# Kernel optimization log

Measured on AMD Instinct MI355X. Metric: run time of the kernel, lower is better.

Reference implementation:

```python
import jax, jax.numpy as jnp
from jax import lax
import numpy as np

B, L, D, MD, H, R, T = 128, 128, 300, 50, 512, 128, 4
HD = H // 2          # per-direction GRU hidden
GIN = D + MD         # GRU input dim (word emb + mask emb)


def setup_inputs():
    key = jax.random.key(0)
    ks = jax.random.split(key, 16)
    s = 0.05
    sents = jax.random.normal(ks[0], (B, L, D), jnp.float32)
    lens = jnp.sort(jax.random.randint(ks[1], (B,), 96, L + 1))[::-1]  # sorted desc, like pack_padded
    j = jnp.arange(L)
    # aspect span: positions 5..7 are the target (contiguous ones, inside every lens)
    masks = ((j >= 5) & (j < 8)).astype(jnp.int32)[None, :] * jnp.ones((B, 1), jnp.int32)
    labels = jax.random.randint(ks[2], (B,), 0, 3)
    mask_table = jax.random.normal(ks[3], (2, MD)) * s
    gWihf = jax.random.normal(ks[4], (3 * HD, GIN)) * s
    gWhhf = jax.random.normal(ks[5], (3 * HD, HD)) * s
    gbihf = jnp.zeros((3 * HD,), jnp.float32)
    gbhhf = jnp.zeros((3 * HD,), jnp.float32)
    gWihb = jax.random.normal(ks[6], (3 * HD, GIN)) * s
    gWhhb = jax.random.normal(ks[7], (3 * HD, HD)) * s
    gbihb = jnp.zeros((3 * HD,), jnp.float32)
    gbhhb = jnp.zeros((3 * HD,), jnp.float32)
    hW = jax.random.normal(ks[8], (4, R, H)) * s   # 4 branch hNlinear weights [R,H]
    hb = jnp.zeros((4, R), jnp.float32)
    tW = jax.random.normal(ks[9], (4, T, R)) * s   # 4 branch feat2tri weights [T,R]
    tb = jnp.zeros((4, T), jnp.float32)
    trans = jax.random.normal(ks[10], (4, T, T)) * s  # 4 CRF transition matrices
    lW = jax.random.normal(ks[11], (3, 4 * H)) * s    # feat2label2
    lb = jnp.zeros((3,), jnp.float32)
    return {"sents": sents, "mask_table": mask_table,
            "gWihf": gWihf, "gWhhf": gWhhf, "gbihf": gbihf, "gbhhf": gbhhf,
            "gWihb": gWihb, "gWhhb": gWhhb, "gbihb": gbihb, "gbhhb": gbhhb,
            "hW": hW, "hb": hb, "tW": tW, "tb": tb, "trans": trans,
            "lW": lW, "lb": lb, "masks": masks, "lens": lens, "labels": labels}


def _gru_dir(x, valid, Wih, Whh, bih, bhh):
    # x: [B,L,GIN], valid: [B,L] bool. PyTorch GRU cell; padded steps emit 0 and keep hidden.
    gi_all = jnp.einsum('bld,gd->blg', x, Wih) + bih  # precompute input GEMM [B,L,3HD]

    def step(h, inp):
        gi, m = inp  # [B,3HD], [B]
        gh = h @ Whh.T + bhh
        ir, iz, inn = jnp.split(gi, 3, axis=-1)
        hr, hz, hn = jnp.split(gh, 3, axis=-1)
        r = jax.nn.sigmoid(ir + hr)
        z = jax.nn.sigmoid(iz + hz)
        n = jnp.tanh(inn + r * hn)
        hnew = (1.0 - z) * n + z * h
        h_carry = jnp.where(m[:, None], hnew, h)
        y = jnp.where(m[:, None], hnew, 0.0)
        return h_carry, y

    h0 = jnp.zeros((x.shape[0], HD), x.dtype)
    _, ys = lax.scan(step, h0, (gi_all.transpose(1, 0, 2), valid.T))
    return ys.transpose(1, 0, 2)  # [B,L,HD]


def _crf_marginals(feats, valid, trans):
    # feats: [B,L,T], valid: [B,L] bool, trans: [T,T]. Forward-backward marginals.
    fT = feats.transpose(1, 0, 2)  # [L,B,T]
    mT = valid.T                   # [L,B]

    def fwd(alpha, inp):
        f, m = inp
        new = jax.nn.logsumexp(alpha[:, :, None] + trans[None], axis=1) + f
        alpha = jnp.where(m[:, None], new, alpha)
        return alpha, alpha

    alpha0 = fT[0]
    _, alphas = lax.scan(fwd, alpha0, (fT[1:], mT[1:]))
    alphas = jnp.concatenate([alpha0[None], alphas], axis=0)  # [L,B,T]

    def bwd(beta, inp):
        f_next, m_next = inp
        new = jax.nn.logsumexp(trans[None] + (f_next + beta)[:, None, :], axis=2)
        beta = jnp.where(m_next[:, None], new, beta)
        return beta, beta

    beta_last = jnp.zeros_like(alpha0)
    _, betas = lax.scan(bwd, beta_last, (fT[1:], mT[1:]), reverse=True)
    betas = jnp.concatenate([betas, beta_last[None]], axis=0)  # [L,B,T]
    return jax.nn.softmax(alphas + betas, axis=-1).transpose(1, 0, 2)  # [B,L,T]


def _pos_weights(masks, lens):
    # replicates get_pos_weight
    j = jnp.arange(L)[None, :]
    begin = jnp.argmax(masks, axis=1)[:, None]
    tnum = jnp.sum(masks, axis=1)[:, None]
    lf = lens.astype(jnp.float32)[:, None]
    w = jnp.where(j < begin, 1.0 - (begin - j).astype(jnp.float32) / lf, 0.0)
    w = jnp.where(masks == 1, 1.0, w)
    w = jnp.where(j > begin + tnum, 1.0 - (j - begin).astype(jnp.float32) / lf, w)
    w = jnp.where(j > lens[:, None], 0.0, w)
    return w  # [B,L]


def _model(sents, mask_table, gWihf, gWhhf, gbihf, gbhhf, gWihb, gWhhb, gbihb, gbhhb,
           hW, hb, tW, tb, trans, lW, lb, masks, lens, labels):
    valid = jnp.arange(L)[None, :] < lens[:, None]  # [B,L]
    x = jnp.concatenate([sents, mask_table[masks]], axis=-1)  # [B,L,GIN]

    hf = _gru_dir(x, valid, gWihf, gWhhf, gbihf, gbhhf)
    # backward direction: reverse each sequence within its valid length
    j = jnp.arange(L)[None, :]
    rev_idx = jnp.clip(lens[:, None] - 1 - j, 0, L - 1)  # [B,L]
    x_rev = jnp.take_along_axis(x, rev_idx[:, :, None], axis=1)
    hb_rev = _gru_dir(x_rev, valid, gWihb, gWhhb, gbihb, gbhhb)
    hbk = jnp.take_along_axis(hb_rev, rev_idx[:, :, None], axis=1) * valid[:, :, None]

    ctx = jnp.concatenate([hf, hbk], axis=-1)  # [B,L,H]
    ctx = ctx * _pos_weights(masks, lens)[:, :, None]

    validf = valid.astype(ctx.dtype)
    svs = []
    for k in range(4):
        ck = jnp.einsum('blh,rh->blr', ctx, hW[k]) + hb[k]      # hNlinear
        fk = jnp.einsum('blr,tr->blt', ck, tW[k]) + tb[k]       # feat2triN
        marg = _crf_marginals(fk, valid, trans[k])
        sp = marg[:, :, 1] * validf                              # select tag-1 polarity in valid range
        sp = sp / jnp.sum(sp, axis=1, keepdims=True)             # normalize by gamma
        svs.append(jnp.einsum('bl,blh->bh', sp, ctx))            # weighted pooling

    sv = jax.nn.relu(jnp.concatenate(svs, axis=-1))  # [B,4H] (eval: dropout = identity)
    scores = sv @ lW.T + lb                          # [B,3]
    logp = jax.nn.log_softmax(scores, axis=1)
    cls_loss = -jnp.mean(logp[jnp.arange(B), labels])
    return cls_loss


def reference(sents, mask_table, gWihf, gWhhf, gbihf, gbhhf, gWihb, gWhhb, gbihb, gbhhb,
              hW, hb, tW, tb, trans, lW, lb, masks, lens, labels):
    return _model(sents, mask_table, gWihf, gWhhf, gbihf, gbhhf, gWihb, gWhhb, gbihb, gbhhb,
                  hW, hb, tW, tb, trans, lW, lb, masks, lens, labels)
```

## Files before the change

### kernel.cpp

```cpp
#include <hip/hip_runtime.h>
#include <hip/hip_bf16.h>

#define BB 128
#define LL 128
#define DD 300
#define MDIM 50
#define GINDIM 350
#define HDIM 256
#define G3 768
#define HH 512
#define RR 128
#define TT 4
#define NKB 4
#define MTOT (BB*LL)
#define N2 1536
#define KP 352

typedef __attribute__((ext_vector_type(8))) short short8;
typedef __attribute__((ext_vector_type(4))) float f32x4;

#define OFF_GI      0ull
#define OFF_CTXB    50331648ull
#define OFF_XBF     67108864ull
#define OFF_WIHB    78643200ull
#define OFF_WHHB    79724544ull
#define OFF_BIAS    80510976ull
#define OFF_W2      80517120ull
#define OFF_B2      80549888ull
#define OFF_BEG     80550144ull
#define OFF_TN      80550656ull
#define OFF_SCORES  80551168ull
#define OFF_FK      80553216ull
#define OFF_AL      81601792ull
#define OFF_SP      82650368ull
#define OFF_SPSUM   82912512ull
#define OFF_SV      82914560ull

__device__ __forceinline__ float sig_f(float x) { return 1.f / (1.f + __expf(-x)); }
__device__ __forceinline__ float tanh_f(float x) { float e = __expf(2.f * x); return 1.f - 2.f / (e + 1.f); }
__device__ __forceinline__ float b2f(unsigned short u) { return __uint_as_float(((unsigned)u) << 16); }

__global__ __launch_bounds__(256) void k_zero(float4* p) {
    size_t n4 = 16777216ull / 16;
    for (size_t i = blockIdx.x * 256ull + threadIdx.x; i < n4; i += (size_t)gridDim.x * 256ull)
        p[i] = make_float4(0.f, 0.f, 0.f, 0.f);
}

__global__ __launch_bounds__(256) void k_prep_x(const float* __restrict__ sents,
        const float* __restrict__ mask_table, const int* __restrict__ masks,
        __hip_bfloat16* __restrict__ xbf) {
    int idx = blockIdx.x * 256 + threadIdx.x;
    if (idx >= MTOT * KP) return;
    int m = idx / KP, k = idx % KP;
    float v = 0.f;
    if (k < DD) v = sents[(size_t)m * DD + k];
    else if (k < GINDIM) v = mask_table[masks[m] * MDIM + (k - DD)];
    xbf[idx] = __float2bfloat16(v);
}

__global__ __launch_bounds__(256) void k_prep_wihB(const float* __restrict__ Wf,
        const float* __restrict__ Wb, const float* __restrict__ bf_,
        const float* __restrict__ bb_, __hip_bfloat16* __restrict__ wihB,
        float* __restrict__ biasAll) {
    int idx = blockIdx.x * 256 + threadIdx.x;
    if (idx < N2 * KP) {
        int n = idx / KP, k = idx % KP;
        int dir = n >= G3; int g = n - dir * G3;
        const float* W = dir ? Wb : Wf;
        float v = (k < GINDIM) ? W[(size_t)g * GINDIM + k] : 0.f;
        wihB[idx] = __float2bfloat16(v);
    }
    if (idx < N2) biasAll[idx] = (idx < G3) ? bf_[idx] : bb_[idx - G3];
}

__global__ __launch_bounds__(256) void k_prep_whhB(const float* __restrict__ Wf,
        const float* __restrict__ Wb, __hip_bfloat16* __restrict__ whhB) {
    int idx = blockIdx.x * 256 + threadIdx.x;
    if (idx >= 2 * G3 * HDIM) return;
    int dir = idx / (G3 * HDIM);
    const float* W = dir ? Wb : Wf;
    whhB[idx] = __float2bfloat16(W[idx - dir * G3 * HDIM]);
}

__global__ __launch_bounds__(256) void k_prep_w2(const float* __restrict__ hW,
        const float* __restrict__ hb, const float* __restrict__ tW,
        const float* __restrict__ tb, float* __restrict__ W2, float* __restrict__ b2) {
    int idx = blockIdx.x * 256 + threadIdx.x;
    if (idx < 16 * HH) {
        int kt = idx >> 9, h = idx & 511;
        int k = kt >> 2, t = kt & 3;
        const float* tw = tW + (size_t)(k * TT + t) * RR;
        const float* hw = hW + (size_t)k * RR * HH + h;
        float acc = 0.f;
        #pragma unroll 4
        for (int r = 0; r < RR; ++r) acc += tw[r] * hw[(size_t)r * HH];
        W2[idx] = acc;
    }
    if (idx < 16) {
        int k = idx >> 2, t = idx & 3;
        const float* tw = tW + (size_t)(k * TT + t) * RR;
        const float* hbk = hb + k * RR;
        float acc = tb[k * TT + t];
        for (int r = 0; r < RR; ++r) acc += tw[r] * hbk[r];
        b2[idx] = acc;
    }
}

__global__ __launch_bounds__(128) void k_prep_bt(const int* __restrict__ masks,
        int* __restrict__ beg, int* __restrict__ tn) {
    int b = threadIdx.x;
    int best = masks[b * LL]; int idx = 0; int s = 0;
    for (int j = 0; j < LL; ++j) {
        int v = masks[b * LL + j]; s += v;
        if (v > best) { best = v; idx = j; }
    }
    beg[b] = idx; tn[b] = s;
}

__global__ __launch_bounds__(256) void k_mfma_gi(const short* __restrict__ xbf,
        const short* __restrict__ wihB, const float* __restrict__ biasAll,
        __hip_bfloat16* __restrict__ gi) {
    __shared__ short As[64][40];
    __shared__ short Bs[64][40];
    const int tid = threadIdx.x;
    const int m0 = blockIdx.y * 64, n0 = blockIdx.x * 64;
    const int w = tid >> 6, lane = tid & 63;
    const int srow = tid >> 2, skc = (tid & 3) * 8;
    const int frow = lane & 15, fkc = (lane >> 4) * 8;
    const int rb = (w >> 1) * 32, cb = (w & 1) * 32;
    f32x4 zero = {0.f, 0.f, 0.f, 0.f};
    f32x4 acc[2][2] = {zero, zero, zero, zero};
    for (int k0 = 0; k0 < KP; k0 += 32) {
        *(short8*)&As[srow][skc] = *(const short8*)&xbf[(size_t)(m0 + srow) * KP + k0 + skc];
        *(short8*)&Bs[srow][skc] = *(const short8*)&wihB[(size_t)(n0 + srow) * KP + k0 + skc];
        __syncthreads();
        short8 a[2], b[2];
        #pragma unroll
        for (int i = 0; i < 2; ++i) a[i] = *(const short8*)&As[rb + i * 16 + frow][fkc];
        #pragma unroll
        for (int j = 0; j < 2; ++j) b[j] = *(const short8*)&Bs[cb + j * 16 + frow][fkc];
        #pragma unroll
        for (int i = 0; i < 2; ++i)
            #pragma unroll
            for (int j = 0; j < 2; ++j)
                acc[i][j] = __builtin_amdgcn_mfma_f32_16x16x32_bf16(a[i], b[j], acc[i][j], 0, 0, 0);
        __syncthreads();
    }
    #pragma unroll
    for (int i = 0; i < 2; ++i) {
        #pragma unroll
        for (int j = 0; j < 2; ++j) {
            int col = n0 + cb + j * 16 + frow;
            int dir = col >= G3; int g = col - dir * G3;
            float bias = biasAll[col];
            #pragma unroll
            for (int r = 0; r < 4; ++r) {
                int m = m0 + rb + i * 16 + (lane >> 4) * 4 + r;
                gi[((size_t)dir * MTOT + m) * G3 + g] = __float2bfloat16(acc[i][j][r] + bias);
            }
        }
    }
}

__device__ __forceinline__ float poswt(int j, int beg, int tn, int len, float lf, int mv) {
    float w = (j < beg) ? (1.f - (float)(beg - j) / lf) : 0.f;
    if (mv == 1) w = 1.f;
    if (j > beg + tn) w = 1.f - (float)(j - beg) / lf;
    if (j > len) w = 0.f;
    return w;
}

__global__ __launch_bounds__(512, 1) void k_gru_mfma(
        const __hip_bfloat16* __restrict__ gi, const short* __restrict__ whhB,
        const float* __restrict__ gbhhf, const float* __restrict__ gbhhb,
        const int* __restrict__ lens, const int* __restrict__ masks,
        const int* __restrict__ beg_, const int* __restrict__ tn_,
        __hip_bfloat16* __restrict__ ctxb) {
    __shared__ short hA[16][264];
    __shared__ float gates[16][772];
    __shared__ float s_w[16][128];
    __shared__ int s_len[16];
    __shared__ int s_maxlen;

    const int tid = threadIdx.x;
    const int w = tid >> 6, lane = tid & 63;
    const int dir = blockIdx.x >> 3, grp = blockIdx.x & 7;
    const int b0 = grp * 16;
    const int frow = lane & 15, fkc = (lane >> 4) * 8;
    const int colg = w * 96;

    if (tid < 16) s_len[tid] = lens[b0 + tid];
    for (int e = tid; e < 16 * 264; e += 512) ((short*)hA)[e] = 0;
    __syncthreads();
    if (tid == 0) {
        int m = 0;
        #pragma unroll
        for (int q = 0; q < 16; ++q) m = max(m, s_len[q]);
        s_maxlen = m;
    }
    for (int e = tid; e < 16 * 128; e += 512) {
        int bl = e >> 7, j = e & 127;
        int b = b0 + bl;
        int len = s_len[bl];
        s_w[bl][j] = poswt(j, beg_[b], tn_[b], len, (float)len, masks[b * LL + j]);
    }

    short8 bu[48];
    #pragma unroll
    for (int ct = 0; ct < 6; ++ct)
        #pragma unroll
        for (int kk = 0; kk < 8; ++kk)
            bu[ct * 8 + kk] = *(const short8*)&whhB[((size_t)dir * G3 + colg + ct * 16 + frow) * HDIM + kk * 32 + fkc];

    const int i_idx = tid & 255;
    const int bbase = (tid >> 8) * 8;
    const float* bhh = dir ? gbhhb : gbhhf;
    const float bhr = bhh[i_idx], bhz = bhh[HDIM + i_idx], bhn = bhh[2 * HDIM + i_idx];
    const unsigned short* giD = (const unsigned short*)gi + (size_t)dir * MTOT * G3;
    float hv[8];
    #pragma unroll
    for (int q = 0; q < 8; ++q) hv[q] = 0.f;
    __syncthreads();

    const int maxlen = s_maxlen;
    const f32x4 zero = {0.f, 0.f, 0.f, 0.f};
    for (int l = 0; l < maxlen; ++l) {
        unsigned short g0[8], g1[8], g2[8];
        #pragma unroll
        for (int q = 0; q < 8; ++q) {
            int bl = bbase + q;
            int len = s_len[bl];
            int pos = dir ? (len - 1 - l) : l;
            if (l >= len) pos = 0;
            const unsigned short* grow = giD + ((size_t)(b0 + bl) * LL + pos) * G3 + i_idx;
            g0[q] = grow[0];
            g1[q] = grow[HDIM];
            g2[q] = grow[2 * HDIM];
        }
        f32x4 acc[6];
        #pragma unroll
        for (int ct = 0; ct < 6; ++ct) acc[ct] = zero;
        #pragma unroll
        for (int kk = 0; kk < 8; ++kk) {
            short8 a = *(const short8*)&hA[frow][kk * 32 + fkc];
            #pragma unroll
            for (int ct = 0; ct < 6; ++ct)
                acc[ct] = __builtin_amdgcn_mfma_f32_16x16x32_bf16(a, bu[ct * 8 + kk], acc[ct], 0, 0, 0);
        }
        #pragma unroll
        for (int ct = 0; ct < 6; ++ct) {
            int col = colg + ct * 16 + frow;
            #pragma unroll
            for (int r = 0; r < 4; ++r)
                gates[(lane >> 4) * 4 + r][col] = acc[ct][r];
        }
        __syncthreads();
        #pragma unroll
        for (int q = 0; q < 8; ++q) {
            int bl = bbase + q;
            int len = s_len[bl];
            bool valid = l < len;
            int pos = dir ? (len - 1 - l) : l;
            if (!valid) pos = 0;
            float rr = sig_f(b2f(g0[q]) + gates[bl][i_idx] + bhr);
            float zz = sig_f(b2f(g1[q]) + gates[bl][HDIM + i_idx] + bhz);
            float nn = tanh_f(b2f(g2[q]) + rr * (gates[bl][2 * HDIM + i_idx] + bhn));
            float h = (1.f - zz) * nn + zz * hv[q];
            if (valid) {
                hv[q] = h;
                __hip_bfloat16 hb16 = __float2bfloat16(h);
                hA[bl][i_idx] = *reinterpret_cast<short*>(&hb16);
                float hw = h * s_w[bl][pos];
                ctxb[((size_t)(b0 + bl) * LL + pos) * HH + dir * HDIM + i_idx] = __float2bfloat16(hw);
            }
        }
        __syncthreads();
    }
}

__global__ __launch_bounds__(256) void k_fk(const __hip_bfloat16* __restrict__ ctxb,
        const float* __restrict__ W2, const float* __restrict__ b2,
        float* __restrict__ fk) {
    int gid = blockIdx.x * 256 + threadIdx.x;
    int m = gid >> 4, kt = gid & 15;
    const short8* crow = (const short8*)((const short*)ctxb + (size_t)m * HH);
    const float* w2 = W2 + kt * HH;
    float acc = b2[kt];
    #pragma unroll 4
    for (int c = 0; c < HH / 8; ++c) {
        short8 v = crow[c];
        #pragma unroll
        for (int j = 0; j < 8; ++j)
            acc += b2f((unsigned short)v[j]) * w2[c * 8 + j];
    }
    fk[((size_t)(kt >> 2) * MTOT + m) * TT + (kt & 3)] = acc;
}

__global__ __launch_bounds__(64) void k_crf(const float* __restrict__ fk,
        const float* __restrict__ trans, const int* __restrict__ lens,
        float* __restrict__ alphas, float* __restrict__ sp, float* __restrict__ spsum) {
    const int tid = blockIdx.x * 64 + threadIdx.x;
    const int pid = tid >> 2;
    const int t = tid & 3;
    const int k = pid >> 7, b = pid & 127;
    const int len = lens[b];
    const float* f = fk + ((size_t)k * MTOT + (size_t)b * LL) * TT;
    const float* tr = trans + k * 16;
    const float trC0 = tr[0 * 4 + t], trC1 = tr[1 * 4 + t], trC2 = tr[2 * 4 + t], trC3 = tr[3 * 4 + t];
    const float trR0 = tr[t * 4 + 0], trR1 = tr[t * 4 + 1], trR2 = tr[t * 4 + 2], trR3 = tr[t * 4 + 3];
    float* al = alphas + ((size_t)k * BB + b) * LL * TT;
    const int base = threadIdx.x & ~3;
    float alpha = f[t];
    al[t] = alpha;
    for (int l = 1; l < LL; ++l) {
        float a0 = __shfl(alpha, base + 0);
        float a1 = __shfl(alpha, base + 1);
        float a2 = __shfl(alpha, base + 2);
        float a3 = __shfl(alpha, base + 3);
        float v0 = a0 + trC0, v1 = a1 + trC1, v2 = a2 + trC2, v3 = a3 + trC3;
        float mx = fmaxf(fmaxf(v0, v1), fmaxf(v2, v3));
        float sum = __expf(v0 - mx) + __expf(v1 - mx) + __expf(v2 - mx) + __expf(v3 - mx);
        float nw = mx + __logf(sum) + f[l * TT + t];
        if (l < len) alpha = nw;
        al[l * TT + t] = alpha;
    }
    float beta = 0.f;
    float ssum = 0.f;
    for (int l = LL - 1; l >= 0; --l) {
        if (l < LL - 1) {
            float fb = f[(l + 1) * TT + t] + beta;
            float c0 = __shfl(fb, base + 0);
            float c1 = __shfl(fb, base + 1);
            float c2 = __shfl(fb, base + 2);
            float c3 = __shfl(fb, base + 3);
            float w0 = trR0 + c0, w1 = trR1 + c1, w2 = trR2 + c2, w3 = trR3 + c3;
            float mx = fmaxf(fmaxf(w0, w1), fmaxf(w2, w3));
            float nb = mx + __logf(__expf(w0 - mx) + __expf(w1 - mx) + __expf(w2 - mx) + __expf(w3 - mx));
            if (l + 1 < len) beta = nb;
        }
        float v = al[l * TT + t] + beta;
        float mx = fmaxf(v, __shfl_xor(v, 1));
        mx = fmaxf(mx, __shfl_xor(mx, 2));
        float p = __expf(v - mx);
        float s = p;
        s += __shfl_xor(s, 1);
        s += __shfl_xor(s, 2);
        float m1 = __shfl(p, base + 1) / s;
        float spv = (l < len) ? m1 : 0.f;
        if (t == 0) sp[((size_t)k * BB + b) * LL + l] = spv;
        ssum += spv;
    }
    if (t == 0) spsum[k * BB + b] = ssum;
}

__global__ __launch_bounds__(256) void k_pool(const __hip_bfloat16* __restrict__ ctxb,
        const float* __restrict__ sp, const float* __restrict__ spsum,
        float* __restrict__ sv) {
    __shared__ float s_sp[NKB][LL];
    __shared__ float s_inv[NKB];
    const int b = blockIdx.x;
    const int tid = threadIdx.x;
    for (int i = tid; i < NKB * LL; i += 256) {
        int k = i >> 7, l = i & 127;
        s_sp[k][l] = sp[((size_t)k * BB + b) * LL + l];
    }
    if (tid < NKB) s_inv[tid] = 1.f / spsum[tid * BB + b];
    __syncthreads();
    const int n0 = tid * 8;
    const int k = n0 >> 9, h0 = n0 & 511;
    float acc[8] = {};
    const short* cb = (const short*)ctxb;
    for (int l = 0; l < LL; ++l) {
        float spl = s_sp[k][l];
        short8 v = *(const short8*)&cb[((size_t)b * LL + l) * HH + h0];
        #pragma unroll
        for (int j = 0; j < 8; ++j)
            acc[j] += spl * b2f((unsigned short)v[j]);
    }
    float inv = s_inv[k];
    #pragma unroll
    for (int j = 0; j < 8; ++j)
        sv[(size_t)b * 2048 + n0 + j] = acc[j] * inv;
}

__global__ __launch_bounds__(256) void k_scores(const float* __restrict__ sv,
        const float* __restrict__ lW, const float* __restrict__ lb,
        float* __restrict__ scores) {
    __shared__ float red[3][4];
    const int b = blockIdx.x;
    const int tid = threadIdx.x;
    const float* svb = sv + (size_t)b * 2048;
    float a0 = 0.f, a1 = 0.f, a2 = 0.f;
    for (int i = tid; i < 2048; i += 256) {
        float v = fmaxf(svb[i], 0.f);
        a0 += v * lW[i];
        a1 += v * lW[2048 + i];
        a2 += v * lW[4096 + i];
    }
    #pragma unroll
    for (int off = 32; off > 0; off >>= 1) {
        a0 += __shfl_down(a0, off);
        a1 += __shfl_down(a1, off);
        a2 += __shfl_down(a2, off);
    }
    const int wid = tid >> 6, lane = tid & 63;
    if (lane == 0) { red[0][wid] = a0; red[1][wid] = a1; red[2][wid] = a2; }
    __syncthreads();
    if (tid < 3) {
        scores[b * 3 + tid] = red[tid][0] + red[tid][1] + red[tid][2] + red[tid][3] + lb[tid];
    }
}

__global__ __launch_bounds__(128) void k_final2(const float* __restrict__ scores,
        const int* __restrict__ labels, float* __restrict__ out) {
    __shared__ float red[128];
    const int b = threadIdx.x;
    float s0 = scores[b * 3 + 0], s1 = scores[b * 3 + 1], s2 = scores[b * 3 + 2];
    float mx = fmaxf(s0, fmaxf(s1, s2));
    float lse = mx + logf(expf(s0 - mx) + expf(s1 - mx) + expf(s2 - mx));
    int lab = labels[b];
    float sc = lab == 0 ? s0 : (lab == 1 ? s1 : s2);
    red[b] = lse - sc;
    __syncthreads();
    for (int st = 64; st > 0; st >>= 1) {
        if (b < st) red[b] += red[b + st];
        __syncthreads();
    }
    if (b == 0) out[0] = red[0] * (1.f / 128.f);
}

extern "C" void kernel_launch(void* const* d_in, const int* in_sizes, int n_in,
                              void* d_out, int out_size, void* d_ws, size_t ws_size,
                              hipStream_t stream) {
    const float* sents      = (const float*)d_in[0];
    const float* mask_table = (const float*)d_in[1];
    const float* gWihf      = (const float*)d_in[2];
    const float* gWhhf      = (const float*)d_in[3];
    const float* gbihf      = (const float*)d_in[4];
    const float* gbhhf      = (const float*)d_in[5];
    const float* gWihb      = (const float*)d_in[6];
    const float* gWhhb      = (const float*)d_in[7];
    const float* gbihb      = (const float*)d_in[8];
    const float* gbhhb      = (const float*)d_in[9];
    const float* hW         = (const float*)d_in[10];
    const float* hb         = (const float*)d_in[11];
    const float* tW         = (const float*)d_in[12];
    const float* tb         = (const float*)d_in[13];
    const float* trans      = (const float*)d_in[14];
    const float* lW         = (const float*)d_in[15];
    const float* lb         = (const float*)d_in[16];
    const int*   masks      = (const int*)d_in[17];
    const int*   lens       = (const int*)d_in[18];
    const int*   labels     = (const int*)d_in[19];

    char* wsb = (char*)d_ws;
    __hip_bfloat16* gi    = (__hip_bfloat16*)(wsb + OFF_GI);
    __hip_bfloat16* ctxb  = (__hip_bfloat16*)(wsb + OFF_CTXB);
    __hip_bfloat16* xbf   = (__hip_bfloat16*)(wsb + OFF_XBF);
    __hip_bfloat16* wihB  = (__hip_bfloat16*)(wsb + OFF_WIHB);
    __hip_bfloat16* whhB  = (__hip_bfloat16*)(wsb + OFF_WHHB);
    float* biasAll        = (float*)(wsb + OFF_BIAS);
    float* W2             = (float*)(wsb + OFF_W2);
    float* b2             = (float*)(wsb + OFF_B2);
    int* beg              = (int*)(wsb + OFF_BEG);
    int* tn               = (int*)(wsb + OFF_TN);
    float* scores         = (float*)(wsb + OFF_SCORES);
    float* fk             = (float*)(wsb + OFF_FK);
    float* alphas         = (float*)(wsb + OFF_AL);
    float* sp             = (float*)(wsb + OFF_SP);
    float* spsum          = (float*)(wsb + OFF_SPSUM);
    float* sv             = (float*)(wsb + OFF_SV);

    hipLaunchKernelGGL(k_zero, dim3(1024), dim3(256), 0, stream, (float4*)(wsb + OFF_CTXB));
    hipLaunchKernelGGL(k_prep_x, dim3((MTOT * KP + 255) / 256), dim3(256), 0, stream,
                       sents, mask_table, masks, xbf);
    hipLaunchKernelGGL(k_prep_wihB, dim3((N2 * KP + 255) / 256), dim3(256), 0, stream,
                       gWihf, gWihb, gbihf, gbihb, wihB, biasAll);
    hipLaunchKernelGGL(k_prep_whhB, dim3((2 * G3 * HDIM + 255) / 256), dim3(256), 0, stream,
                       gWhhf, gWhhb, whhB);
    hipLaunchKernelGGL(k_prep_w2, dim3((16 * HH + 255) / 256), dim3(256), 0, stream,
                       hW, hb, tW, tb, W2, b2);
    hipLaunchKernelGGL(k_prep_bt, dim3(1), dim3(128), 0, stream, masks, beg, tn);

    hipLaunchKernelGGL(k_mfma_gi, dim3(N2 / 64, MTOT / 64), dim3(256), 0, stream,
                       (const short*)xbf, (const short*)wihB, biasAll, gi);
    hipLaunchKernelGGL(k_gru_mfma, dim3(16), dim3(512), 0, stream,
                       gi, (const short*)whhB, gbhhf, gbhhb, lens, masks, beg, tn, ctxb);
    hipLaunchKernelGGL(k_fk, dim3(MTOT * 16 / 256), dim3(256), 0, stream,
                       ctxb, W2, b2, fk);
    hipLaunchKernelGGL(k_crf, dim3(32), dim3(64), 0, stream, fk, trans, lens, alphas, sp, spsum);
    hipLaunchKernelGGL(k_pool, dim3(BB), dim3(256), 0, stream, ctxb, sp, spsum, sv);
    hipLaunchKernelGGL(k_scores, dim3(BB), dim3(256), 0, stream, sv, lW, lb, scores);
    hipLaunchKernelGGL(k_final2, dim3(1), dim3(128), 0, stream, scores, labels, (float*)d_out);
}
```

Measured before the change: 970.2 us.

## Prefetch GRU input gates into LDS with async double buffering

The recurrent GRU kernel now stages the next timestep's precomputed input-gate rows into a double-buffered LDS area using global_load_lds, instead of issuing per-thread global loads on the critical path each step. The r and z hidden biases are folded into the precomputed input bias so they no longer need adding in the loop. The recurrent weight fragments are held in named registers through macros, and the waves-per-EU attribute is changed. The intent is to hide global memory latency in this serial 128-step loop, at the cost of about 48KB of extra LDS. One risk is that no explicit vmcnt wait guards the async LDS writes before they are read.

```diff
diff --git a/kernel.cpp b/kernel.cpp
--- a/kernel.cpp
+++ b/kernel.cpp
@@ -40,6 +40,11 @@
 __device__ __forceinline__ float tanh_f(float x) { float e = __expf(2.f * x); return 1.f - 2.f / (e + 1.f); }
 __device__ __forceinline__ float b2f(unsigned short u) { return __uint_as_float(((unsigned)u) << 16); }
 
+__device__ __forceinline__ void gload_lds16(const void* g, void* l) {
+    __builtin_amdgcn_global_load_lds((const __attribute__((address_space(1))) unsigned int*)g,
+                                     (__attribute__((address_space(3))) unsigned int*)l, 16, 0, 0);
+}
+
 __global__ __launch_bounds__(256) void k_zero(float4* p) {
     size_t n4 = 16777216ull / 16;
     for (size_t i = blockIdx.x * 256ull + threadIdx.x; i < n4; i += (size_t)gridDim.x * 256ull)
@@ -60,7 +65,8 @@
 
 __global__ __launch_bounds__(256) void k_prep_wihB(const float* __restrict__ Wf,
         const float* __restrict__ Wb, const float* __restrict__ bf_,
-        const float* __restrict__ bb_, __hip_bfloat16* __restrict__ wihB,
+        const float* __restrict__ bb_, const float* __restrict__ bhf_,
+        const float* __restrict__ bhb_, __hip_bfloat16* __restrict__ wihB,
         float* __restrict__ biasAll) {
     int idx = blockIdx.x * 256 + threadIdx.x;
     if (idx < N2 * KP) {
@@ -70,7 +76,12 @@
         float v = (k < GINDIM) ? W[(size_t)g * GINDIM + k] : 0.f;
         wihB[idx] = __float2bfloat16(v);
     }
-    if (idx < N2) biasAll[idx] = (idx < G3) ? bf_[idx] : bb_[idx - G3];
+    if (idx < N2) {
+        int dir = idx >= G3; int g = idx - dir * G3;
+        float v = dir ? bb_[g] : bf_[g];
+        if (g < 2 * HDIM) v += dir ? bhb_[g] : bhf_[g];
+        biasAll[idx] = v;
+    }
 }
 
 __global__ __launch_bounds__(256) void k_prep_whhB(const float* __restrict__ Wf,
@@ -170,15 +181,51 @@
     return w;
 }
 
-__global__ __launch_bounds__(512, 1) void k_gru_mfma(
-        const __hip_bfloat16* __restrict__ gi, const short* __restrict__ whhB,
+#define LB(ct,kk) const short8 bu_##ct##_##kk = *(const short8*)(wB + (ct * 16) * HDIM + (kk) * 32);
+#define LBCT(ct) LB(ct,0) LB(ct,1) LB(ct,2) LB(ct,3) LB(ct,4) LB(ct,5) LB(ct,6) LB(ct,7)
+#define MM(kk) { const short8 a = *(const short8*)(aB + (kk) * 32); \
+    acc0 = __builtin_amdgcn_mfma_f32_16x16x32_bf16(a, bu_0_##kk, acc0, 0, 0, 0); \
+    acc1 = __builtin_amdgcn_mfma_f32_16x16x32_bf16(a, bu_1_##kk, acc1, 0, 0, 0); \
+    acc2 = __builtin_amdgcn_mfma_f32_16x16x32_bf16(a, bu_2_##kk, acc2, 0, 0, 0); \
+    acc3 = __builtin_amdgcn_mfma_f32_16x16x32_bf16(a, bu_3_##kk, acc3, 0, 0, 0); \
+    acc4 = __builtin_amdgcn_mfma_f32_16x16x32_bf16(a, bu_4_##kk, acc4, 0, 0, 0); \
+    acc5 = __builtin_amdgcn_mfma_f32_16x16x32_bf16(a, bu_5_##kk, acc5, 0, 0, 0); }
+#define GW(ct) { const int col = colg + ct * 16 + frow; \
+    gates[r0 + 0][col] = acc##ct[0]; gates[r0 + 1][col] = acc##ct[1]; \
+    gates[r0 + 2][col] = acc##ct[2]; gates[r0 + 3][col] = acc##ct[3]; }
+#define NQ(q, hvq) { \
+    const int bl = bbase + q; \
+    const int len = s_len[bl]; \
+    const bool valid = l < len; \
+    int pos = dir ? (len - 1 - l) : l; \
+    if (!valid) pos = 0; \
+    const short* gb = &giLds[(l & 1) * 12288 + bl * 768]; \
+    float gvr = b2f((unsigned short)gb[i_idx]); \
+    float gvz = b2f((unsigned short)gb[256 + i_idx]); \
+    float gvn = b2f((unsigned short)gb[512 + i_idx]); \
+    float rr = sig_f(gvr + gates[bl][i_idx]); \
+    float zz = sig_f(gvz + gates[bl][HDIM + i_idx]); \
+    float nn = tanh_f(gvn + rr * (gates[bl][2 * HDIM + i_idx] + bhn)); \
+    float h = (1.f - zz) * nn + zz * hvq; \
+    if (valid) { \
+        hvq = h; \
+        __hip_bfloat16 hb16 = __float2bfloat16(h); \
+        hA[bl][i_idx] = *(short*)&hb16; \
+        float hw = h * s_w[bl][pos]; \
+        ctxb[((size_t)(b0 + bl) * LL + pos) * HH + dirH + i_idx] = __float2bfloat16(hw); \
+    } }
+
+__global__ __launch_bounds__(512) __attribute__((amdgpu_waves_per_eu(2, 2)))
+void k_gru_mfma(
+        const short* __restrict__ gi, const short* __restrict__ whhB,
         const float* __restrict__ gbhhf, const float* __restrict__ gbhhb,
         const int* __restrict__ lens, const int* __restrict__ masks,
         const int* __restrict__ beg_, const int* __restrict__ tn_,
         __hip_bfloat16* __restrict__ ctxb) {
+    __shared__ float gates[16][772];
     __shared__ short hA[16][264];
-    __shared__ float gates[16][772];
     __shared__ float s_w[16][128];
+    __shared__ short giLds[2 * 12288];
     __shared__ int s_len[16];
     __shared__ int s_maxlen;
 
@@ -188,6 +235,8 @@
     const int b0 = grp * 16;
     const int frow = lane & 15, fkc = (lane >> 4) * 8;
     const int colg = w * 96;
+    const int r0 = (lane >> 4) * 4;
+    const int dirH = dir * HDIM;
 
     if (tid < 16) s_len[tid] = lens[b0 + tid];
     for (int e = tid; e < 16 * 264; e += 512) ((short*)hA)[e] = 0;
@@ -205,75 +254,43 @@
         s_w[bl][j] = poswt(j, beg_[b], tn_[b], len, (float)len, masks[b * LL + j]);
     }
 
-    short8 bu[48];
-    #pragma unroll
-    for (int ct = 0; ct < 6; ++ct)
-        #pragma unroll
-        for (int kk = 0; kk < 8; ++kk)
-            bu[ct * 8 + kk] = *(const short8*)&whhB[((size_t)dir * G3 + colg + ct * 16 + frow) * HDIM + kk * 32 + fkc];
+    const short* wB = whhB + ((size_t)dir * G3 + colg + frow) * HDIM + fkc;
+    LBCT(0) LBCT(1) LBCT(2) LBCT(3) LBCT(4) LBCT(5)
 
     const int i_idx = tid & 255;
     const int bbase = (tid >> 8) * 8;
-    const float* bhh = dir ? gbhhb : gbhhf;
-    const float bhr = bhh[i_idx], bhz = bhh[HDIM + i_idx], bhn = bhh[2 * HDIM + i_idx];
-    const unsigned short* giD = (const unsigned short*)gi + (size_t)dir * MTOT * G3;
-    float hv[8];
-    #pragma unroll
-    for (int q = 0; q < 8; ++q) hv[q] = 0.f;
+    const float bhn = (dir ? gbhhb : gbhhf)[2 * HDIM + i_idx];
+    const short* giD = gi + (size_t)dir * MTOT * G3;
+    const short* aB = &hA[frow][fkc];
+    float hv0 = 0.f, hv1 = 0.f, hv2 = 0.f, hv3 = 0.f, hv4 = 0.f, hv5 = 0.f, hv6 = 0.f, hv7 = 0.f;
     __syncthreads();
-
     const int maxlen = s_maxlen;
+
+    auto stage = [&](int ll, int bsel) {
+        #pragma unroll
+        for (int j = 0; j < 3; ++j) {
+            int flat = j * 512 + tid;
+            int bl = flat / 96;
+            int off16 = flat - bl * 96;
+            int len = s_len[bl];
+            int pos = dir ? (len - 1 - ll) : ll;
+            if (ll >= len) pos = 0;
+            const char* src = (const char*)giD + ((size_t)((b0 + bl) * LL + pos) * G3 + off16 * 8) * 2;
+            short* dst = &giLds[bsel * 12288 + (j * 512 + (tid & ~63)) * 8];
+            gload_lds16(src, dst);
+        }
+    };
+    stage(0, 0);
+
     const f32x4 zero = {0.f, 0.f, 0.f, 0.f};
     for (int l = 0; l < maxlen; ++l) {
-        unsigned short g0[8], g1[8], g2[8];
-        #pragma unroll
-        for (int q = 0; q < 8; ++q) {
-            int bl = bbase + q;
-            int len = s_len[bl];
-            int pos = dir ? (len - 1 - l) : l;
-            if (l >= len) pos = 0;
-            const unsigned short* grow = giD + ((size_t)(b0 + bl) * LL + pos) * G3 + i_idx;
-            g0[q] = grow[0];
-            g1[q] = grow[HDIM];
-            g2[q] = grow[2 * HDIM];
-        }
-        f32x4 acc[6];
-        #pragma unroll
-        for (int ct = 0; ct < 6; ++ct) acc[ct] = zero;
-        #pragma unroll
-        for (int kk = 0; kk < 8; ++kk) {
-            short8 a = *(const short8*)&hA[frow][kk * 32 + fkc];
-            #pragma unroll
-            for (int ct = 0; ct < 6; ++ct)
-                acc[ct] = __builtin_amdgcn_mfma_f32_16x16x32_bf16(a, bu[ct * 8 + kk], acc[ct], 0, 0, 0);
-        }
-        #pragma unroll
-        for (int ct = 0; ct < 6; ++ct) {
-            int col = colg + ct * 16 + frow;
-            #pragma unroll
-            for (int r = 0; r < 4; ++r)
-                gates[(lane >> 4) * 4 + r][col] = acc[ct][r];
-        }
+        if (l + 1 < maxlen) stage(l + 1, (l + 1) & 1);
+        f32x4 acc0 = zero, acc1 = zero, acc2 = zero, acc3 = zero, acc4 = zero, acc5 = zero;
+        MM(0) MM(1) MM(2) MM(3) MM(4) MM(5) MM(6) MM(7)
+        GW(0) GW(1) GW(2) GW(3) GW(4) GW(5)
         __syncthreads();
-        #pragma unroll
-        for (int q = 0; q < 8; ++q) {
-            int bl = bbase + q;
-            int len = s_len[bl];
-            bool valid = l < len;
-            int pos = dir ? (len - 1 - l) : l;
-            if (!valid) pos = 0;
-            float rr = sig_f(b2f(g0[q]) + gates[bl][i_idx] + bhr);
-            float zz = sig_f(b2f(g1[q]) + gates[bl][HDIM + i_idx] + bhz);
-            float nn = tanh_f(b2f(g2[q]) + rr * (gates[bl][2 * HDIM + i_idx] + bhn));
-            float h = (1.f - zz) * nn + zz * hv[q];
-            if (valid) {
-                hv[q] = h;
-                __hip_bfloat16 hb16 = __float2bfloat16(h);
-                hA[bl][i_idx] = *reinterpret_cast<short*>(&hb16);
-                float hw = h * s_w[bl][pos];
-                ctxb[((size_t)(b0 + bl) * LL + pos) * HH + dir * HDIM + i_idx] = __float2bfloat16(hw);
-            }
-        }
+        NQ(0, hv0) NQ(1, hv1) NQ(2, hv2) NQ(3, hv3)
+        NQ(4, hv4) NQ(5, hv5) NQ(6, hv6) NQ(7, hv7)
         __syncthreads();
     }
 }
@@ -475,7 +492,7 @@
     hipLaunchKernelGGL(k_prep_x, dim3((MTOT * KP + 255) / 256), dim3(256), 0, stream,
                        sents, mask_table, masks, xbf);
     hipLaunchKernelGGL(k_prep_wihB, dim3((N2 * KP + 255) / 256), dim3(256), 0, stream,
-                       gWihf, gWihb, gbihf, gbihb, wihB, biasAll);
+                       gWihf, gWihb, gbihf, gbihb, gbhhf, gbhhb, wihB, biasAll);
     hipLaunchKernelGGL(k_prep_whhB, dim3((2 * G3 * HDIM + 255) / 256), dim3(256), 0, stream,
                        gWhhf, gWhhb, whhB);
     hipLaunchKernelGGL(k_prep_w2, dim3((16 * HH + 255) / 256), dim3(256), 0, stream,
@@ -485,7 +502,7 @@
     hipLaunchKernelGGL(k_mfma_gi, dim3(N2 / 64, MTOT / 64), dim3(256), 0, stream,
                        (const short*)xbf, (const short*)wihB, biasAll, gi);
     hipLaunchKernelGGL(k_gru_mfma, dim3(16), dim3(512), 0, stream,
-                       gi, (const short*)whhB, gbhhf, gbhhb, lens, masks, beg, tn, ctxb);
+                       (const short*)gi, (const short*)whhB, gbhhf, gbhhb, lens, masks, beg, tn, ctxb);
     hipLaunchKernelGGL(k_fk, dim3(MTOT * 16 / 256), dim3(256), 0, stream,
                        ctxb, W2, b2, fk);
     hipLaunchKernelGGL(k_crf, dim3(32), dim3(64), 0, stream, fk, trans, lens, alphas, sp, spsum);
```

Result: slower. 1.119 ms (+15.3%).
